# Kernel tuning notes

Measured on AMD Instinct MI355X. Metric: run time of the kernel, lower is better.

The kernel has to match this reference:

```python
import jax, jax.numpy as jnp
import numpy as np

DIM = 180
HEADS = 6
WIN = 12
NGS = 2304          # num_gs_seed -> gs len
SQ = 48             # sqrt(num_gs_seed)
B = 64              # window-batch
TABLE = (2 * max(SQ, WIN) - 1) ** 2  # 9025 rows in bias table


def _rel_pos_index():
    # Mirrors the torch __init__ buffer construction (np.unique gives the
    # deterministic sorted-unique indexing the original intends).
    cs = (np.indices((SQ, SQ)) + 0.5) * WIN          # [2, SQ, SQ]
    ct = (np.indices((WIN, WIN)) + 0.5) * SQ
    d = cs.reshape(2, -1)[:, :, None] - ct.reshape(2, -1)[:, None, :]
    _, inv = np.unique(d.flatten(), return_inverse=True)
    idx = inv.reshape(d.shape).astype(np.int64)
    idx[0] *= idx.max()
    return jnp.asarray(idx.sum(0), dtype=jnp.int32)


def setup_inputs() -> dict:
    key = jax.random.key(0)
    ks = jax.random.split(key, 12)
    std = 0.02
    d = DIM
    inp = {
        "gs": jax.random.normal(ks[0], (B, NGS, d), dtype=jnp.float32),
        "feat": jax.random.normal(ks[1], (B, WIN * WIN, d), dtype=jnp.float32),
        "Wq": jax.random.normal(ks[2], (d, d), dtype=jnp.float32) * std,
        "bq": jnp.zeros((d,), dtype=jnp.float32),
        "Wk": jax.random.normal(ks[3], (d, d), dtype=jnp.float32) * std,
        "bk": jnp.zeros((d,), dtype=jnp.float32),
        "Wv": jax.random.normal(ks[4], (d, d), dtype=jnp.float32) * std,
        "bv": jnp.zeros((d,), dtype=jnp.float32),
        "Wp": jax.random.normal(ks[5], (d, d), dtype=jnp.float32) * std,
        "bp": jnp.zeros((d,), dtype=jnp.float32),
        "bias_table": jax.random.normal(ks[6], (TABLE, HEADS), dtype=jnp.float32) * std,
        "rel_pos_index": _rel_pos_index(),
    }
    return inp


def reference(gs, feat, Wq, bq, Wk, bk, Wv, bv, Wp, bp, bias_table, rel_pos_index):
    b, ng, c = gs.shape
    n = feat.shape[1]
    hd = c // HEADS
    scale = hd ** (-0.5)

    q = (gs @ Wq + bq).reshape(b, ng, HEADS, hd).transpose(0, 2, 1, 3) * scale  # [b,H,ng,hd]
    k = (feat @ Wk + bk).reshape(b, n, HEADS, hd).transpose(0, 2, 1, 3)          # [b,H,n,hd]
    v = (feat @ Wv + bv).reshape(b, n, HEADS, hd).transpose(0, 2, 1, 3)

    attn = jnp.einsum('bhqd,bhkd->bhqk', q, k)                                    # [b,H,ng,n]
    bias = bias_table[rel_pos_index]                                              # [ng,n,H]
    attn = attn + jnp.transpose(bias, (2, 0, 1))[None]                            # broadcast over b
    attn = jax.nn.softmax(attn, axis=-1)

    x = jnp.einsum('bhqk,bhkd->bhqd', attn, v)                                    # [b,H,ng,hd]
    x = x.transpose(0, 2, 1, 3).reshape(b, ng, c)
    return x @ Wp + bp
```

## Files before the change

kernel.cpp:

```cpp
#include <hip/hip_runtime.h>

#define DIM   180
#define HEADS 6
#define HD    30
#define NKEY  144
#define NGS   2304
#define BATCH 64
#define TQ    64
#define QT    36
#define WPAD  192
#define SXS   200
#define SPS   144
#define KROW  32
#define VROW  144
#define KB_STRIDE (NKEY * KROW)
#define VB_STRIDE (32 * VROW)

typedef unsigned short u16;
typedef short v8s __attribute__((ext_vector_type(8)));
typedef float v4f __attribute__((ext_vector_type(4)));

__device__ __forceinline__ float bf2f(u16 u) {
    union { unsigned int i; float f; } w; w.i = ((unsigned int)u) << 16; return w.f;
}
__device__ __forceinline__ u16 f2bf(float f) {
    union { float f; unsigned int i; } w; w.f = f;
    unsigned int r = w.i + 0x7fffu + ((w.i >> 16) & 1u);
    return (u16)(r >> 16);
}
__device__ __forceinline__ unsigned cvt_pk_bf16(float lo, float hi) {
    unsigned r;
    asm("v_cvt_pk_bf16_f32 %0, %1, %2" : "=v"(r) : "v"(lo), "v"(hi));
    return r;
}
__device__ __forceinline__ uint2 pack4(const v4f& x) {
    return make_uint2(cvt_pk_bf16(x[0], x[1]), cvt_pk_bf16(x[2], x[3]));
}
__device__ __forceinline__ void gload_lds16(const u16* g, u16* l) {
    __builtin_amdgcn_global_load_lds(
        (const __attribute__((address_space(1))) unsigned int*)g,
        (__attribute__((address_space(3))) unsigned int*)l, 16, 0, 0);
}


__global__ __launch_bounds__(256) void wt_prep_kernel(
    const float* __restrict__ Wq, const float* __restrict__ Wp,
    u16* __restrict__ WqT, u16* __restrict__ WpT) {
    int idx = blockIdx.x * 256 + threadIdx.x;
    int sel = idx >= WPAD * WPAD;
    int rr  = sel ? idx - WPAD * WPAD : idx;
    int j = rr / WPAD, k = rr - j * WPAD;
    float v;
    if (!sel) {
        v = (j < DIM && k < DIM) ? Wq[k * DIM + j] : 0.f;
        WqT[j * WPAD + k] = f2bf(v);
    } else {
        int h = k >> 5, dd = k & 31;
        v = (j < DIM && dd < HD) ? Wp[(h * HD + dd) * DIM + j] : 0.f;
        WpT[j * WPAD + k] = f2bf(v);
    }
}

__global__ __launch_bounds__(256) void gather_bias_kernel(
    const float* __restrict__ table, const int* __restrict__ rpi,
    u16* __restrict__ biasCT) {
    const float LOG2E = 1.4426950408889634f;
    int i = blockIdx.x * 256 + threadIdx.x;
    int lane = i & 63;
    int tile = i >> 6;
    int t = tile % 9;
    int rem = tile / 9;
    int g = rem % 144;
    int h = rem / 144;
    int q  = 16 * g + (lane & 15);
    int n0 = 16 * t + (lane >> 4) * 4;
    const int4 rr = *(const int4*)&rpi[q * NKEY + n0];
    unsigned lo = (unsigned)f2bf(table[rr.x * HEADS + h] * LOG2E) |
                  ((unsigned)f2bf(table[rr.y * HEADS + h] * LOG2E) << 16);
    unsigned hi = (unsigned)f2bf(table[rr.z * HEADS + h] * LOG2E) |
                  ((unsigned)f2bf(table[rr.w * HEADS + h] * LOG2E) << 16);
    ((uint2*)biasCT)[i] = make_uint2(lo, hi);
}

__global__ __launch_bounds__(256) void kv_proj_kernel(
    const float* __restrict__ feat,
    const float* __restrict__ Wk, const float* __restrict__ bk,
    const float* __restrict__ Wv, const float* __restrict__ bv,
    u16* __restrict__ Kb, u16* __restrict__ VbT) {
    __shared__ float sF[16 * DIM];
    int b  = blockIdx.x / 9;
    int n0 = (blockIdx.x % 9) * 16;
    int tid = threadIdx.x;
    {
        const float4* src = (const float4*)(feat + (size_t)(b * NKEY + n0) * DIM);
        float4* dst = (float4*)sF;
        for (int i = tid; i < 16 * 45; i += 256) dst[i] = src[i];
    }
    __syncthreads();
    int j = tid;
    if (j < DIM) {
        float ak[16], av[16];
#pragma unroll
        for (int r = 0; r < 16; ++r) { ak[r] = 0.f; av[r] = 0.f; }
        const float4* sF4 = (const float4*)sF;
        for (int kc = 0; kc < 45; ++kc) {
            int kk = kc * 4;
            float wk0 = Wk[(kk + 0) * DIM + j], wk1 = Wk[(kk + 1) * DIM + j];
            float wk2 = Wk[(kk + 2) * DIM + j], wk3 = Wk[(kk + 3) * DIM + j];
            float wv0 = Wv[(kk + 0) * DIM + j], wv1 = Wv[(kk + 1) * DIM + j];
            float wv2 = Wv[(kk + 2) * DIM + j], wv3 = Wv[(kk + 3) * DIM + j];
#pragma unroll
            for (int r = 0; r < 16; ++r) {
                float4 g = sF4[r * 45 + kc];
                ak[r] = fmaf(g.x, wk0, ak[r]); ak[r] = fmaf(g.y, wk1, ak[r]);
                ak[r] = fmaf(g.z, wk2, ak[r]); ak[r] = fmaf(g.w, wk3, ak[r]);
                av[r] = fmaf(g.x, wv0, av[r]); av[r] = fmaf(g.y, wv1, av[r]);
                av[r] = fmaf(g.z, wv2, av[r]); av[r] = fmaf(g.w, wv3, av[r]);
            }
        }
        int h = j / HD, d = j - HD * h;
        u16* kp = Kb  + (size_t)(b * HEADS + h) * KB_STRIDE;
        u16* vp = VbT + (size_t)(b * HEADS + h) * VB_STRIDE;
        float bkj = bk[j], bvj = bv[j];
#pragma unroll
        for (int r = 0; r < 16; ++r) {
            kp[(n0 + r) * KROW + d] = f2bf(ak[r] + bkj);
            vp[d * VROW + n0 + r]   = f2bf(av[r] + bvj);
        }
    }
}

__global__ __launch_bounds__(256, 3) void attn_kernel(
    const float* __restrict__ gs,
    const u16* __restrict__ WqT, const float* __restrict__ bq,
    const u16* __restrict__ WpT, const float* __restrict__ bp,
    const u16* __restrict__ Kb, const u16* __restrict__ VbT,
    const u16* __restrict__ biasCT, float* __restrict__ out) {

    __shared__ u16 sXQ[TQ * SXS];
    __shared__ u16 sV[32 * VROW];
    __shared__ u16 sPK[TQ * SPS];

    const int tid  = threadIdx.x;
    const int w    = tid >> 6;
    const int lane = tid & 63;
    const int l15  = tid & 15;
    const int quad = (tid >> 4) & 3;
    const int bid  = blockIdx.x;
    const int i8   = bid >> 3;
    const int qt   = i8 >> 3;
    const int b    = (bid & 7) * 8 + (i8 & 7);
    const int q0   = qt * TQ;
    const float SCALE = 0.18257418583505536f * 1.4426950408889634f;

    {
        const float4* src = (const float4*)(gs + (size_t)(b * NGS + q0) * DIM);
        for (int i = tid; i < TQ * 45; i += 256) {
            int row = i / 45, c = i - row * 45;
            float4 g = src[row * 45 + c];
            *(uint2*)&sXQ[row * SXS + c * 4] =
                make_uint2(cvt_pk_bf16(g.x, g.y), cvt_pk_bf16(g.z, g.w));
        }
        for (int i = tid; i < TQ * 16; i += 256)
            sXQ[(i >> 4) * SXS + 180 + (i & 15)] = 0;
    }
    __syncthreads();

    v4f qacc[12];
#pragma unroll
    for (int i = 0; i < 12; ++i) qacc[i] = (v4f){0.f, 0.f, 0.f, 0.f};
    for (int kt = 0; kt < 6; ++kt) {
        v8s A[4];
#pragma unroll
        for (int m = 0; m < 4; ++m)
            A[m] = *(const v8s*)&sXQ[(16 * m + l15) * SXS + kt * 32 + quad * 8];
#pragma unroll
        for (int jj = 0; jj < 3; ++jj) {
            v8s B = *(const v8s*)&WqT[(size_t)((3 * w + jj) * 16 + l15) * WPAD +
                                      kt * 32 + quad * 8];
#pragma unroll
            for (int m = 0; m < 4; ++m)
                qacc[jj * 4 + m] = __builtin_amdgcn_mfma_f32_16x16x32_bf16(
                    A[m], B, qacc[jj * 4 + m], 0, 0, 0);
        }
    }
    __syncthreads();
#pragma unroll
    for (int jj = 0; jj < 3; ++jj) {
        int j = (3 * w + jj) * 16 + l15;
        if (j < DIM) {
            int h = j / HD;
            int pos = j + 2 * h;
            float bqj = bq[j];
#pragma unroll
            for (int m = 0; m < 4; ++m)
#pragma unroll
                for (int r = 0; r < 4; ++r) {
                    float v = (qacc[jj * 4 + m][r] + bqj) * SCALE;
                    sXQ[(16 * m + quad * 4 + r) * SXS + pos] =
                        (u16)cvt_pk_bf16(v, v);
                }
        }
    }
    for (int i = tid; i < TQ * 12; i += 256) {
        int row = i / 12, c = i - row * 12;
        sXQ[row * SXS + (c >> 1) * 32 + 30 + (c & 1)] = 0;
    }
    __syncthreads();

    for (int h = 0; h < HEADS; ++h) {
        if (h) __syncthreads();

        {
            const u16* kg = Kb  + (size_t)(b * HEADS + h) * KB_STRIDE;
            const u16* vg = VbT + (size_t)(b * HEADS + h) * VB_STRIDE;
            for (int i = tid; i < 576; i += 256) gload_lds16(kg + i * 8, sPK + i * 8);
            for (int i = tid; i < 576; i += 256) gload_lds16(vg + i * 8, sV + i * 8);
        }
        const u16* bgt = biasCT +
            ((size_t)((h * 144 + (qt * 4 + w)) * 9) * 256) + lane * 4;
        uint2 bb[9];
#pragma unroll
        for (int t = 0; t < 9; ++t) bb[t] = *(const uint2*)(bgt + t * 256);

        v8s qa = *(const v8s*)&sXQ[(16 * w + l15) * SXS + h * 32 + quad * 8];

        __syncthreads();

        v4f la[9];
#pragma unroll
        for (int t = 0; t < 9; ++t) {
            la[t][0] = bf2f((u16)(bb[t].x & 0xffff));
            la[t][1] = bf2f((u16)(bb[t].x >> 16));
            la[t][2] = bf2f((u16)(bb[t].y & 0xffff));
            la[t][3] = bf2f((u16)(bb[t].y >> 16));
        }
#pragma unroll
        for (int t = 0; t < 9; ++t) {
            v8s kb = *(const v8s*)&sPK[(16 * t + l15) * KROW + quad * 8];
            la[t] = __builtin_amdgcn_mfma_f32_16x16x32_bf16(kb, qa, la[t], 0, 0, 0);
        }

        __syncthreads();

        float m = la[0][0];
#pragma unroll
        for (int t = 0; t < 9; ++t)
#pragma unroll
            for (int r = 0; r < 4; ++r) m = fmaxf(m, la[t][r]);
        m = fmaxf(m, __shfl_xor(m, 16));
        m = fmaxf(m, __shfl_xor(m, 32));
        float s = 0.f;
#pragma unroll
        for (int t = 0; t < 9; ++t)
#pragma unroll
            for (int r = 0; r < 4; ++r) {
                la[t][r] = __builtin_amdgcn_exp2f(la[t][r] - m);
                s += la[t][r];
            }
        s += __shfl_xor(s, 16);
        s += __shfl_xor(s, 32);
        float inv = 1.f / s;

#pragma unroll
        for (int t = 0; t < 9; ++t)
            *(uint2*)&sPK[(16 * w + l15) * SPS + 16 * t + quad * 4] =
                make_uint2(cvt_pk_bf16(la[t][0], la[t][1]),
                           cvt_pk_bf16(la[t][2], la[t][3]));

        v4f x0 = (v4f){0.f, 0.f, 0.f, 0.f}, x1 = x0;
#pragma unroll
        for (int kt = 0; kt < 5; ++kt) {
            v8s pa = (v8s){0, 0, 0, 0, 0, 0, 0, 0};
            v8s a0 = pa, a1 = pa;
            if (!(kt == 4 && quad >= 2)) {
                int co = kt * 32 + quad * 8;
                pa = *(const v8s*)&sPK[(16 * w + l15) * SPS + co];
                a0 = *(const v8s*)&sV[l15 * VROW + co];
                a1 = *(const v8s*)&sV[(16 + l15) * VROW + co];
            }
            x0 = __builtin_amdgcn_mfma_f32_16x16x32_bf16(a0, pa, x0, 0, 0, 0);
            x1 = __builtin_amdgcn_mfma_f32_16x16x32_bf16(a1, pa, x1, 0, 0, 0);
        }
        v4f y0, y1;
#pragma unroll
        for (int r = 0; r < 4; ++r) { y0[r] = x0[r] * inv; y1[r] = x1[r] * inv; }
        *(uint2*)&sXQ[(16 * w + l15) * SXS + h * 32 + quad * 4]      = pack4(y0);
        *(uint2*)&sXQ[(16 * w + l15) * SXS + h * 32 + 16 + quad * 4] = pack4(y1);
    }
    __syncthreads();

    {
        v4f acc[12];
#pragma unroll
        for (int i = 0; i < 12; ++i) acc[i] = (v4f){0.f, 0.f, 0.f, 0.f};
        for (int kt = 0; kt < 6; ++kt) {
            v8s A[4];
#pragma unroll
            for (int m = 0; m < 4; ++m)
                A[m] = *(const v8s*)&sXQ[(16 * m + l15) * SXS + kt * 32 + quad * 8];
#pragma unroll
            for (int jj = 0; jj < 3; ++jj) {
                v8s B = *(const v8s*)&WpT[(size_t)((3 * w + jj) * 16 + l15) * WPAD +
                                          kt * 32 + quad * 8];
#pragma unroll
                for (int m = 0; m < 4; ++m)
                    acc[jj * 4 + m] = __builtin_amdgcn_mfma_f32_16x16x32_bf16(
                        A[m], B, acc[jj * 4 + m], 0, 0, 0);
            }
        }
#pragma unroll
        for (int jj = 0; jj < 3; ++jj) {
            int j = (3 * w + jj) * 16 + l15;
            if (j < DIM) {
                float bpj = bp[j];
#pragma unroll
                for (int m = 0; m < 4; ++m)
#pragma unroll
                    for (int r = 0; r < 4; ++r)
                        out[(size_t)(b * NGS + q0 + 16 * m + quad * 4 + r) * DIM + j] =
                            acc[jj * 4 + m][r] + bpj;
            }
        }
    }
}

extern "C" void kernel_launch(void* const* d_in, const int* in_sizes, int n_in,
                              void* d_out, int out_size, void* d_ws, size_t ws_size,
                              hipStream_t stream) {
    const float* gs    = (const float*)d_in[0];
    const float* feat  = (const float*)d_in[1];
    const float* Wq    = (const float*)d_in[2];
    const float* bq    = (const float*)d_in[3];
    const float* Wk    = (const float*)d_in[4];
    const float* bk    = (const float*)d_in[5];
    const float* Wv    = (const float*)d_in[6];
    const float* bv    = (const float*)d_in[7];
    const float* Wp    = (const float*)d_in[8];
    const float* bp    = (const float*)d_in[9];
    const float* table = (const float*)d_in[10];
    const int*   rpi   = (const int*)d_in[11];
    float* out = (float*)d_out;

    u16* WqT    = (u16*)d_ws;
    u16* WpT    = WqT + WPAD * WPAD;
    u16* Kb     = WpT + WPAD * WPAD;
    u16* VbT    = Kb  + (size_t)BATCH * HEADS * KB_STRIDE;
    u16* biasCT = VbT + (size_t)BATCH * HEADS * VB_STRIDE;

    size_t zero_bytes = (size_t)BATCH * HEADS * (KB_STRIDE + VB_STRIDE) * sizeof(u16);
    hipMemsetAsync(Kb, 0, zero_bytes, stream);

    wt_prep_kernel<<<dim3(2 * WPAD * WPAD / 256), dim3(256), 0, stream>>>(Wq, Wp, WqT, WpT);
    gather_bias_kernel<<<dim3(HEADS * 144 * 9 * 64 / 256), dim3(256), 0, stream>>>(
        table, rpi, biasCT);
    kv_proj_kernel<<<dim3(BATCH * 9), dim3(256), 0, stream>>>(feat, Wk, bk, Wv, bv, Kb, VbT);
    attn_kernel<<<dim3(BATCH * QT), dim3(256), 0, stream>>>(
        gs, WqT, bq, WpT, bp, Kb, VbT, biasCT, out);
}
```

Measured before the change: 365.3 us.

## Keep softmax probabilities in registers via permlane swap and double-buffer K tiles

The attention loop no longer writes softmax probabilities to LDS and reads them back. Instead it builds the PV MFMA operand in registers with v_permlane32_swap, permuting the bias and K layouts to match. K tiles are double-buffered so the next heads' K and V are prefetched after each head, and K rows are XOR-swizzled to avoid LDS bank conflicts. The max and sum reductions become trees, which shortens dependency chains. The cost is more registers and coupled layout permutations across three kernels that must all stay consistent.

```diff
diff --git a/kernel.cpp b/kernel.cpp
--- a/kernel.cpp
+++ b/kernel.cpp
@@ -10,9 +10,8 @@
 #define QT    36
 #define WPAD  192
 #define SXS   200
-#define SPS   144
 #define KROW  32
-#define VROW  144
+#define VROW  152
 #define KB_STRIDE (NKEY * KROW)
 #define VB_STRIDE (32 * VROW)
 
@@ -72,8 +71,10 @@
     int rem = tile / 9;
     int g = rem % 144;
     int h = rem / 144;
+    int qd = (lane >> 4) & 3;
+    int pg = ((qd & 1) << 1) | (qd >> 1);
     int q  = 16 * g + (lane & 15);
-    int n0 = 16 * t + (lane >> 4) * 4;
+    int n0 = 16 * t + pg * 4;
     const int4 rr = *(const int4*)&rpi[q * NKEY + n0];
     unsigned lo = (unsigned)f2bf(table[rr.x * HEADS + h] * LOG2E) |
                   ((unsigned)f2bf(table[rr.y * HEADS + h] * LOG2E) << 16);
@@ -124,8 +125,11 @@
         float bkj = bk[j], bvj = bv[j];
 #pragma unroll
         for (int r = 0; r < 16; ++r) {
-            kp[(n0 + r) * KROW + d] = f2bf(ak[r] + bkj);
-            vp[d * VROW + n0 + r]   = f2bf(av[r] + bvj);
+            int sr = ((r >> 2) == 1) ? r + 4 : ((r >> 2) == 2) ? r - 4 : r;
+            int nn = n0 + sr;
+            kp[nn * KROW + ((((d >> 3) ^ (nn & 3)) & 3) << 3) + (d & 7)] =
+                f2bf(ak[r] + bkj);
+            vp[d * VROW + n0 + r] = f2bf(av[r] + bvj);
         }
     }
 }
@@ -138,8 +142,8 @@
     const u16* __restrict__ biasCT, float* __restrict__ out) {
 
     __shared__ u16 sXQ[TQ * SXS];
+    __shared__ u16 sK2[2 * NKEY * KROW];
     __shared__ u16 sV[32 * VROW];
-    __shared__ u16 sPK[TQ * SPS];
 
     const int tid  = threadIdx.x;
     const int w    = tid >> 6;
@@ -206,17 +210,21 @@
         int row = i / 12, c = i - row * 12;
         sXQ[row * SXS + (c >> 1) * 32 + 30 + (c & 1)] = 0;
     }
+
+    {
+        const u16* kg0 = Kb + (size_t)(b * HEADS + 0) * KB_STRIDE;
+        const u16* kg1 = Kb + (size_t)(b * HEADS + 1) * KB_STRIDE;
+        const u16* vg0 = VbT + (size_t)(b * HEADS + 0) * VB_STRIDE;
+        for (int i = tid; i < 576; i += 256) gload_lds16(kg0 + i * 8, sK2 + i * 8);
+        for (int i = tid; i < 576; i += 256)
+            gload_lds16(kg1 + i * 8, sK2 + NKEY * KROW + i * 8);
+        for (int i = tid; i < 608; i += 256) gload_lds16(vg0 + i * 8, sV + i * 8);
+    }
     __syncthreads();
 
     for (int h = 0; h < HEADS; ++h) {
-        if (h) __syncthreads();
-
-        {
-            const u16* kg = Kb  + (size_t)(b * HEADS + h) * KB_STRIDE;
-            const u16* vg = VbT + (size_t)(b * HEADS + h) * VB_STRIDE;
-            for (int i = tid; i < 576; i += 256) gload_lds16(kg + i * 8, sPK + i * 8);
-            for (int i = tid; i < 576; i += 256) gload_lds16(vg + i * 8, sV + i * 8);
-        }
+        const u16* sKc = sK2 + (h & 1) * (NKEY * KROW);
+
         const u16* bgt = biasCT +
             ((size_t)((h * 144 + (qt * 4 + w)) * 9) * 256) + lane * 4;
         uint2 bb[9];
@@ -224,8 +232,6 @@
         for (int t = 0; t < 9; ++t) bb[t] = *(const uint2*)(bgt + t * 256);
 
         v8s qa = *(const v8s*)&sXQ[(16 * w + l15) * SXS + h * 32 + quad * 8];
-
-        __syncthreads();
 
         v4f la[9];
 #pragma unroll
@@ -237,56 +243,84 @@
         }
 #pragma unroll
         for (int t = 0; t < 9; ++t) {
-            v8s kb = *(const v8s*)&sPK[(16 * t + l15) * KROW + quad * 8];
+            v8s kb = *(const v8s*)&sKc[(16 * t + l15) * KROW +
+                                       ((quad ^ (l15 & 3)) << 3)];
             la[t] = __builtin_amdgcn_mfma_f32_16x16x32_bf16(kb, qa, la[t], 0, 0, 0);
         }
 
-        __syncthreads();
-
-        float m = la[0][0];
+        float mt[9];
 #pragma unroll
         for (int t = 0; t < 9; ++t)
-#pragma unroll
-            for (int r = 0; r < 4; ++r) m = fmaxf(m, la[t][r]);
+            mt[t] = fmaxf(fmaxf(la[t][0], la[t][1]), fmaxf(la[t][2], la[t][3]));
+        float m = fmaxf(fmaxf(fmaxf(fmaxf(mt[0], mt[1]), fmaxf(mt[2], mt[3])),
+                              fmaxf(fmaxf(mt[4], mt[5]), fmaxf(mt[6], mt[7]))),
+                        mt[8]);
         m = fmaxf(m, __shfl_xor(m, 16));
         m = fmaxf(m, __shfl_xor(m, 32));
-        float s = 0.f;
-#pragma unroll
-        for (int t = 0; t < 9; ++t)
-#pragma unroll
-            for (int r = 0; r < 4; ++r) {
+        float st[9];
+#pragma unroll
+        for (int t = 0; t < 9; ++t) {
+#pragma unroll
+            for (int r = 0; r < 4; ++r)
                 la[t][r] = __builtin_amdgcn_exp2f(la[t][r] - m);
-                s += la[t][r];
-            }
+            st[t] = (la[t][0] + la[t][1]) + (la[t][2] + la[t][3]);
+        }
+        float s = (((st[0] + st[1]) + (st[2] + st[3])) +
+                   ((st[4] + st[5]) + (st[6] + st[7]))) + st[8];
         s += __shfl_xor(s, 16);
         s += __shfl_xor(s, 32);
         float inv = 1.f / s;
 
-#pragma unroll
-        for (int t = 0; t < 9; ++t)
-            *(uint2*)&sPK[(16 * w + l15) * SPS + 16 * t + quad * 4] =
-                make_uint2(cvt_pk_bf16(la[t][0], la[t][1]),
-                           cvt_pk_bf16(la[t][2], la[t][3]));
+        unsigned sd0[9], sd1[9];
+#pragma unroll
+        for (int t = 0; t < 9; ++t) {
+            sd0[t] = cvt_pk_bf16(la[t][0], la[t][1]);
+            sd1[t] = cvt_pk_bf16(la[t][2], la[t][3]);
+        }
+
+        __syncthreads();
 
         v4f x0 = (v4f){0.f, 0.f, 0.f, 0.f}, x1 = x0;
 #pragma unroll
         for (int kt = 0; kt < 5; ++kt) {
-            v8s pa = (v8s){0, 0, 0, 0, 0, 0, 0, 0};
-            v8s a0 = pa, a1 = pa;
-            if (!(kt == 4 && quad >= 2)) {
-                int co = kt * 32 + quad * 8;
-                pa = *(const v8s*)&sPK[(16 * w + l15) * SPS + co];
-                a0 = *(const v8s*)&sV[l15 * VROW + co];
-                a1 = *(const v8s*)&sV[(16 + l15) * VROW + co];
-            }
-            x0 = __builtin_amdgcn_mfma_f32_16x16x32_bf16(a0, pa, x0, 0, 0, 0);
-            x1 = __builtin_amdgcn_mfma_f32_16x16x32_bf16(a1, pa, x1, 0, 0, 0);
+            unsigned d0, d1, d2, d3;
+            if (kt < 4) {
+                d0 = sd0[2 * kt];     d1 = sd1[2 * kt];
+                d2 = sd0[2 * kt + 1]; d3 = sd1[2 * kt + 1];
+            } else {
+                d0 = sd0[8]; d1 = sd1[8]; d2 = 0u; d3 = 0u;
+            }
+            asm("v_permlane32_swap_b32 %0, %1" : "+v"(d0), "+v"(d2));
+            asm("v_permlane32_swap_b32 %0, %1" : "+v"(d1), "+v"(d3));
+            union { unsigned u[4]; v8s v; } pu;
+            pu.u[0] = d0; pu.u[1] = d1; pu.u[2] = d2; pu.u[3] = d3;
+            int co = kt * 32 + quad * 8;
+            co = (co < NKEY) ? co : 0;
+            v8s a0 = *(const v8s*)&sV[l15 * VROW + co];
+            v8s a1 = *(const v8s*)&sV[(16 + l15) * VROW + co];
+            x0 = __builtin_amdgcn_mfma_f32_16x16x32_bf16(a0, pu.v, x0, 0, 0, 0);
+            x1 = __builtin_amdgcn_mfma_f32_16x16x32_bf16(a1, pu.v, x1, 0, 0, 0);
         }
         v4f y0, y1;
 #pragma unroll
         for (int r = 0; r < 4; ++r) { y0[r] = x0[r] * inv; y1[r] = x1[r] * inv; }
         *(uint2*)&sXQ[(16 * w + l15) * SXS + h * 32 + quad * 4]      = pack4(y0);
         *(uint2*)&sXQ[(16 * w + l15) * SXS + h * 32 + 16 + quad * 4] = pack4(y1);
+
+        if (h < HEADS - 1) {
+            __syncthreads();
+            if (h + 2 < HEADS) {
+                const u16* kg = Kb + (size_t)(b * HEADS + h + 2) * KB_STRIDE;
+                u16* dst = sK2 + (h & 1) * (NKEY * KROW);
+                for (int i = tid; i < 576; i += 256)
+                    gload_lds16(kg + i * 8, dst + i * 8);
+            }
+            {
+                const u16* vg = VbT + (size_t)(b * HEADS + h + 1) * VB_STRIDE;
+                for (int i = tid; i < 608; i += 256)
+                    gload_lds16(vg + i * 8, sV + i * 8);
+            }
+        }
     }
     __syncthreads();
 
```

Result: no change. 361.6 us (-1.0%).
